# Kernel optimization log

Hardware: AMD Instinct MI355X
Metric: run time of the kernel (lower is better)

The kernel has to match this reference:

```python
import jax, jax.numpy as jnp
import numpy as np

D_MODEL = 2048
N_HEADS = 8
N_KV = 4
HEAD_DIM = 256
WINDOW = 1024
EPS = 1e-6
ROPE_BASE = 10000.0


def _rms_norm(x, w):
    # x: [..., D]; matches torch: x * rsqrt(mean(x^2) + eps) * w
    return x * jax.lax.rsqrt(jnp.mean(x * x, axis=-1, keepdims=True) + EPS) * w


def _rope_cos_sin(pos):
    # pos: [T] ints -> cos/sin: [T, HEAD_DIM] (cat(freqs, freqs) as in source)
    inv_freq = 1.0 / (ROPE_BASE ** (jnp.arange(0, HEAD_DIM, 2, dtype=jnp.float32) / HEAD_DIM))
    freqs = pos.astype(jnp.float32)[:, None] * inv_freq[None, :]  # [T, D/2]
    emb = jnp.concatenate([freqs, freqs], axis=-1)                # [T, D]
    return jnp.cos(emb), jnp.sin(emb)


def _apply_rotary(x, cos, sin):
    # x: [B, H, T, D]; interleaved rotate-half exactly as the torch code
    x1 = x[..., 0::2]
    x2 = x[..., 1::2]
    x_rot = jnp.stack([-x2, x1], axis=-1).reshape(x.shape)
    return x * cos[None, None, :, :] + x_rot * sin[None, None, :, :]


def setup_inputs() -> dict:
    key = jax.random.key(0)
    ks = jax.random.split(key, 8)
    B, T = 1, 4096
    s = 0.02
    return {
        "x": jax.random.normal(ks[0], (B, T, D_MODEL), dtype=jnp.float32),
        "pos": jnp.arange(T, dtype=jnp.int32),
        "Wq": jax.random.normal(ks[1], (N_HEADS * HEAD_DIM, D_MODEL), dtype=jnp.float32) * s,
        "Wk": jax.random.normal(ks[2], (N_KV * HEAD_DIM, D_MODEL), dtype=jnp.float32) * s,
        "Wv": jax.random.normal(ks[3], (N_KV * HEAD_DIM, D_MODEL), dtype=jnp.float32) * s,
        "Wo": jax.random.normal(ks[4], (D_MODEL, N_HEADS * HEAD_DIM), dtype=jnp.float32) * s,
        "q_norm_w": jnp.ones((HEAD_DIM,), dtype=jnp.float32),
        "k_norm_w": jnp.ones((HEAD_DIM,), dtype=jnp.float32),
    }


def reference(x, pos, Wq, Wk, Wv, Wo, q_norm_w, k_norm_w):
    B, T, _ = x.shape
    # projections (torch Linear: y = x @ W.T)
    q = (x @ Wq.T).reshape(B, T, N_HEADS, HEAD_DIM).transpose(0, 2, 1, 3)  # [B,H,T,D]
    k = (x @ Wk.T).reshape(B, T, N_KV, HEAD_DIM).transpose(0, 2, 1, 3)    # [B,Hkv,T,D]
    v = (x @ Wv.T).reshape(B, T, N_KV, HEAD_DIM).transpose(0, 2, 1, 3)
    # per-head RMSNorm
    q = _rms_norm(q, q_norm_w)
    k = _rms_norm(k, k_norm_w)
    # RoPE
    cos, sin = _rope_cos_sin(pos)
    q = _apply_rotary(q, cos, sin)
    k = _apply_rotary(k, cos, sin)
    # GQA repeat: [B,Hkv,T,D] -> [B,H,T,D]
    rep = N_HEADS // N_KV
    k = jnp.repeat(k, rep, axis=1)
    v = jnp.repeat(v, rep, axis=1)
    # full scores + sliding-window causal mask (faithful to source)
    scores = jnp.einsum("bhqd,bhkd->bhqk", q, k) / jnp.sqrt(jnp.float32(HEAD_DIM))
    i = jnp.arange(T)[:, None]
    j = jnp.arange(T)[None, :]
    allowed = (j <= i) & (j >= i - WINDOW + 1)  # [T,T]
    scores = jnp.where(allowed[None, None, :, :], scores, -jnp.inf)
    attn = jax.nn.softmax(scores, axis=-1)
    y = jnp.einsum("bhqk,bhkd->bhqd", attn, v)
    y = y.transpose(0, 2, 1, 3).reshape(B, T, N_HEADS * HEAD_DIM)
    return y @ Wo.T
```

## Files before the change

kernel.cpp:

```cpp
#include <hip/hip_runtime.h>
#include <cstdint>
#include <cmath>

typedef __bf16 bf16x8 __attribute__((ext_vector_type(8)));
typedef float  f32x4  __attribute__((ext_vector_type(4)));

#define DEVI __device__ __forceinline__

#define SEQ 4096
#define NH 8
#define NKV 4
#define HD 256
#define WIN 1024

DEVI void gload16(const void* g, void* l) {
  __builtin_amdgcn_global_load_lds((const __attribute__((address_space(1))) void*)g,
                                   (__attribute__((address_space(3))) void*)l,
                                   16, 0, 0);
}

DEVI bf16x8 ld8f(const float* p) {
  const f32x4 a = *(const f32x4*)p;
  const f32x4 b = *(const f32x4*)(p + 4);
  bf16x8 r;
#pragma unroll
  for (int j = 0; j < 4; ++j) { r[j] = (__bf16)a[j]; r[4 + j] = (__bf16)b[j]; }
  return r;
}

DEVI void st1(float* p, float v)  { *p = v; }
DEVI void st1(__bf16* p, float v) { *p = (__bf16)v; }

DEVI void barx() {
  asm volatile("" ::: "memory");
  __builtin_amdgcn_s_barrier();
  asm volatile("" ::: "memory");
}

__global__ __launch_bounds__(256)
void cvt_all(const float* __restrict__ x,  const float* __restrict__ wq,
             const float* __restrict__ wk, const float* __restrict__ wv,
             const float* __restrict__ wo,
             __bf16* __restrict__ xb, __bf16* __restrict__ wqkvb,
             __bf16* __restrict__ wob) {
  const size_t g = (size_t)blockIdx.x * 256 + threadIdx.x;
  const float* src; __bf16* dst; size_t off;
  if      (g < 1048576) { src = x;  dst = xb;               off = g; }
  else if (g < 1572864) { src = wq; dst = wqkvb;            off = g - 1048576; }
  else if (g < 1835008) { src = wk; dst = wqkvb + 4194304;  off = g - 1572864; }
  else if (g < 2097152) { src = wv; dst = wqkvb + 6291456;  off = g - 1835008; }
  else                  { src = wo; dst = wob;              off = g - 2097152; }
  *(bf16x8*)(dst + off * 8) = ld8f(src + off * 8);
}

template <int BM, typename TC>
__global__ __launch_bounds__(512, 2)
void gemm256(const __bf16* __restrict__ A, const __bf16* __restrict__ B,
             TC* __restrict__ C, int N, int K) {
  constexpr int AI    = BM / 128;
  constexpr int MF    = BM / 32;
  constexpr int MH    = MF / 2;
  constexpr int AUNIT = BM * 64;
  constexpr int ASZ   = 4 * AUNIT;
  constexpr int VMC   = 2 * AI + 4;
  __shared__ char lds[ASZ + 65536];

  const int tid  = threadIdx.x;
  const int lane = tid & 63;
  const int wave = tid >> 6;
  const int l15  = lane & 15;
  const int l4   = lane >> 4;
  const int wm   = wave >> 2;
  const int wn   = wave & 3;

  constexpr int nTm = 4096 / BM;
  const int lin  = blockIdx.x;
  const int xcd  = lin & 7;
  const int kk   = lin >> 3;
  const int nTn  = N >> 8;
  const int rowT = kk % nTm;
  const int colT = xcd * (nTn >> 3) + kk / nTm;
  const int row0 = rowT * BM;
  const int col0 = colT << 8;

  const int srow = tid >> 2;
  const int scol = ((tid & 3) ^ ((tid >> 3) & 3)) << 3;
  const __bf16* Asrc = A + (size_t)(row0 + srow) * K + scol;
  const __bf16* Bsrc = B + (size_t)(col0 + srow) * K + scol;

  const int swz  = (l4 ^ ((l15 >> 1) & 3)) << 4;
  const int aoff = (wm * (BM / 2) + l15) * 64 + swz;
  const int boff = ((wn << 6) + l15) * 64 + swz;

  auto stA = [&](int kx, int h) {
    int k0 = kx << 6; if (k0 >= K) k0 = 0;
    const __bf16* s = Asrc + k0 + (h << 5);
    char* d = lds + ((kx & 1) * 2 + h) * AUNIT + wave * 1024;
#pragma unroll
    for (int i = 0; i < AI; ++i)
      gload16(s + (size_t)(i << 7) * K, d + i * 8192);
  };
  auto stB = [&](int kx, int h) {
    int k0 = kx << 6; if (k0 >= K) k0 = 0;
    const __bf16* s = Bsrc + k0 + (h << 5);
    char* d = lds + ASZ + ((kx & 1) * 2 + h) * 16384 + wave * 1024;
#pragma unroll
    for (int i = 0; i < 2; ++i)
      gload16(s + (size_t)(i << 7) * K, d + i * 8192);
  };

  f32x4 acc[MF][4] = {};

  stA(0, 0); stB(0, 0); stA(0, 1); stB(0, 1); stA(1, 0); stB(1, 0);
  asm volatile("s_waitcnt vmcnt(%0)" :: "i"(VMC) : "memory");
  barx();

  const int NT = K >> 6;
  for (int kt = 0; kt < NT; ++kt) {
    const int bb = (kt & 1) * 2;
    bf16x8 bfr[4];
    bf16x8 af[MH];

    auto rd = [&](int h, int mg, bool readB) {
      const char* pa = lds + (bb + h) * AUNIT + aoff;
#pragma unroll
      for (int m = 0; m < MH; ++m)
        af[m] = *(const bf16x8*)(pa + ((mg * MH + m) << 10));
      if (readB) {
        const char* pb = lds + ASZ + (bb + h) * 16384 + boff;
#pragma unroll
        for (int n = 0; n < 4; ++n)
          bfr[n] = *(const bf16x8*)(pb + (n << 10));
      }
    };
    auto mm = [&](int mg) {
      barx();
      __builtin_amdgcn_s_setprio(1);
#pragma unroll
      for (int m = 0; m < MH; ++m)
#pragma unroll
        for (int n = 0; n < 4; ++n)
          acc[mg * MH + m][n] =
              __builtin_amdgcn_mfma_f32_16x16x32_bf16(af[m], bfr[n], acc[mg * MH + m][n], 0, 0, 0);
      __builtin_amdgcn_s_setprio(0);
    };

    rd(0, 0, true);
    stA(kt + 1, 1);
    mm(0);
    rd(0, 1, false);
    stB(kt + 1, 1);
    asm volatile("s_waitcnt vmcnt(%0)" :: "i"(VMC) : "memory");
    mm(1);
    rd(1, 0, true);
    stA(kt + 2, 0);
    mm(0);
    rd(1, 1, false);
    stB(kt + 2, 0);
    asm volatile("s_waitcnt vmcnt(%0)" :: "i"(VMC) : "memory");
    mm(1);
  }
  asm volatile("s_waitcnt vmcnt(0)" ::: "memory");

#pragma unroll
  for (int mf = 0; mf < MF; ++mf) {
    const int rb = row0 + wm * (BM / 2) + (mf >> 2) * 64 + (mf & 3) * 16 + (l4 << 2);
#pragma unroll
    for (int reg = 0; reg < 4; ++reg) {
      TC* crow = C + (size_t)(rb + reg) * N + col0 + (wn << 6) + l15;
#pragma unroll
      for (int n = 0; n < 4; ++n) st1(crow + (n << 4), acc[mf][n][reg]);
    }
  }
}

__global__ __launch_bounds__(256)
void norm_rope_tv(__bf16* __restrict__ qkv, __bf16* __restrict__ Vt,
                  const float* __restrict__ qw, const float* __restrict__ kw,
                  const int* __restrict__ pos) {
  if (blockIdx.x < 12288) {
    const int gw   = blockIdx.x * 4 + (threadIdx.x >> 6);
    const int lane = threadIdx.x & 63;
    __bf16* base; const float* w; int t;
    if (gw < SEQ * NH) {
      t = gw >> 3;
      base = qkv + (size_t)t * 4096 + (gw & 7) * HD;
      w = qw;
    } else {
      const int g = gw - SEQ * NH;
      t = g >> 2;
      base = qkv + (size_t)t * 4096 + 2048 + (g & 3) * HD;
      w = kw;
    }

    const int d0 = lane * 4;
    float v[4]; float ss = 0.f;
#pragma unroll
    for (int j = 0; j < 4; ++j) { v[j] = (float)base[d0 + j]; ss += v[j] * v[j]; }
#pragma unroll
    for (int off = 1; off < 64; off <<= 1) ss += __shfl_xor(ss, off);
    const float rms = rsqrtf(ss * (1.0f / 256.0f) + 1e-6f);
    const float p = (float)pos[t];

    float n[4];
#pragma unroll
    for (int j = 0; j < 4; ++j) n[j] = v[j] * rms * w[d0 + j];

    float outv[4];
#pragma unroll
    for (int e = 0; e < 4; e += 2) {
      const int i0 = d0 + e, i1 = i0 + 1;
      const float f0 = exp2f(-(float)(i0 & 127) * 0.103810253f);
      const float f1 = exp2f(-(float)(i1 & 127) * 0.103810253f);
      float s0, cc0, s1, cc1;
      sincosf(p * f0, &s0, &cc0);
      sincosf(p * f1, &s1, &cc1);
      outv[e]     = n[e] * cc0 - n[e + 1] * s0;
      outv[e + 1] = n[e + 1] * cc1 + n[e] * s1;
    }
#pragma unroll
    for (int j = 0; j < 4; ++j) base[d0 + j] = (__bf16)outv[j];
  } else {
    __shared__ __bf16 tile[64][72];
    const int b   = blockIdx.x - 12288;
    const int tid = threadIdx.x;
    const int tb  = (b & 63) * 64;
    const int yy  = b >> 6;
    const int kvh = yy >> 2;
    const int db  = (yy & 3) * 64;
#pragma unroll
    for (int i = 0; i < 2; ++i) {
      const int s = i * 256 + tid;
      const int r = s >> 3, c = (s & 7) * 8;
      bf16x8 val = *(const bf16x8*)(qkv + (size_t)(tb + r) * 4096 + 3072 + kvh * HD + db + c);
#pragma unroll
      for (int j = 0; j < 8; ++j) tile[r][c + j] = val[j];
    }
    __syncthreads();
#pragma unroll
    for (int i = 0; i < 2; ++i) {
      const int s = i * 256 + tid;
      const int r = s >> 3, c = (s & 7) * 8;
      bf16x8 outv;
#pragma unroll
      for (int j = 0; j < 8; ++j) outv[j] = tile[c + j][r];
      *(bf16x8*)(Vt + (size_t)(kvh * HD + db + r) * SEQ + tb + c) = outv;
    }
  }
}

__global__ __launch_bounds__(256, 2)
void attn_fwd(const __bf16* __restrict__ qkv, const __bf16* __restrict__ Vt,
              __bf16* __restrict__ Y) {
  __shared__ char klds[2][16384];
  __shared__ char vlds[2][16384];
  __shared__ __bf16 Ps[4][16][40];
  const int tid  = threadIdx.x;
  const int lane = tid & 63;
  const int wave = tid >> 6;
  const int l15  = lane & 15;
  const int l4   = lane >> 4;
  const int lin  = blockIdx.x;
  const int head = lin & 7;
  const int q0   = (lin >> 3) * 64;
  const int kvh  = head >> 1;
  const int qw   = q0 + wave * 16;

  bf16x8 qf[8];
  const __bf16* qrow = qkv + (size_t)(qw + l15) * 4096 + head * HD;
#pragma unroll
  for (int ks = 0; ks < 8; ++ks) {
    bf16x8 t = *(const bf16x8*)(qrow + ks * 32 + l4 * 8);
#pragma unroll
    for (int j = 0; j < 8; ++j) t[j] = (__bf16)((float)t[j] * 0.0625f);
    qf[ks] = t;
  }

  f32x4 o[16] = {};
  float l_run[4] = {0.f, 0.f, 0.f, 0.f};

  int lo = q0 - (WIN - 1); if (lo < 0) lo = 0;
  const int kt0 = lo >> 5;
  const int kt1 = (q0 + 63) >> 5;
  const int kbmax = kt1 << 5;

  const int skey = (tid >> 2) & 31;
  const int sdim = tid >> 2;
  const int sg   = (tid & 3) ^ ((tid >> 3) & 3);
  const int sth  = tid >> 7;

  auto stK = [&](int kt, int b) {
    int kb = kt << 5; if (kb > kbmax) kb = kbmax;
    const __bf16* s = qkv + (size_t)(kb + skey) * 4096 + 2048 + kvh * HD
                          + sth * 32 + sg * 8;
    char* d = klds[b] + wave * 1024;
#pragma unroll
    for (int i = 0; i < 4; ++i)
      gload16(s + i * 64, d + i * 4096);
  };
  auto stV = [&](int kt, int b) {
    int kb = kt << 5; if (kb > kbmax) kb = kbmax;
    const __bf16* s = Vt + ((size_t)kvh * HD + sdim) * SEQ + kb + sg * 8;
    char* d = vlds[b] + wave * 1024;
#pragma unroll
    for (int i = 0; i < 4; ++i)
      gload16(s + (size_t)i * 64 * SEQ, d + i * 4096);
  };

  stK(kt0, 0);     stV(kt0, 0);
  stK(kt0 + 1, 1); stV(kt0 + 1, 1);

  const int rswz = (l4 ^ ((l15 >> 1) & 3)) << 4;

  for (int kt = kt0; kt <= kt1; ++kt) {
    const int p  = (kt - kt0) & 1;
    const int kb = kt << 5;
    asm volatile("s_waitcnt vmcnt(8)" ::: "memory");
    barx();

    const char* kbase = klds[p];
    f32x4 s_acc[2] = {};
    __builtin_amdgcn_s_setprio(1);
#pragma unroll
    for (int kn = 0; kn < 2; ++kn) {
#pragma unroll
      for (int ks = 0; ks < 8; ++ks) {
        bf16x8 kf = *(const bf16x8*)(kbase + (ks * 32 + kn * 16 + l15) * 64 + rswz);
        s_acc[kn] = __builtin_amdgcn_mfma_f32_16x16x32_bf16(qf[ks], kf, s_acc[kn], 0, 0, 0);
      }
    }
    __builtin_amdgcn_s_setprio(0);

#pragma unroll
    for (int reg = 0; reg < 4; ++reg) {
      const int r  = l4 * 4 + reg;
      const int qg = qw + r;
      float ps = 0.f;
#pragma unroll
      for (int kn = 0; kn < 2; ++kn) {
        const int kg = kb + kn * 16 + l15;
        const bool ok = (kg <= qg) && (kg > qg - WIN);
        const float pv = ok ? __expf(fminf(s_acc[kn][reg], 34.f) - 34.f) : 0.f;
        ps += pv;
        Ps[wave][r][kn * 16 + l15] = (__bf16)pv;
      }
      l_run[reg] += ps;
    }

    const char* vbase = vlds[p];
    bf16x8 pf = *(const bf16x8*)&Ps[wave][l15][l4 * 8];
    __builtin_amdgcn_s_setprio(1);
#pragma unroll
    for (int dn = 0; dn < 16; ++dn) {
      bf16x8 vf = *(const bf16x8*)(vbase + (dn * 16 + l15) * 64 + rswz);
      o[dn] = __builtin_amdgcn_mfma_f32_16x16x32_bf16(pf, vf, o[dn], 0, 0, 0);
    }
    __builtin_amdgcn_s_setprio(0);

    barx();
    stK(kt + 2, p);
    stV(kt + 2, p);
  }
  asm volatile("s_waitcnt vmcnt(0)" ::: "memory");

#pragma unroll
  for (int reg = 0; reg < 4; ++reg) {
#pragma unroll
    for (int off = 1; off < 16; off <<= 1)
      l_run[reg] += __shfl_xor(l_run[reg], off);
    const float inv = 1.0f / l_run[reg];
    const int q = qw + l4 * 4 + reg;
    __bf16* yrow = Y + ((size_t)q * NH + head) * HD + l15;
#pragma unroll
    for (int dn = 0; dn < 16; ++dn)
      yrow[dn * 16] = (__bf16)(o[dn][reg] * inv);
  }
}

extern "C" void kernel_launch(void* const* d_in, const int* in_sizes, int n_in,
                              void* d_out, int out_size, void* d_ws, size_t ws_size,
                              hipStream_t stream) {
  (void)in_sizes; (void)n_in; (void)out_size; (void)ws_size;
  const float* x   = (const float*)d_in[0];
  const int*   pos = (const int*)d_in[1];
  const float* Wq  = (const float*)d_in[2];
  const float* Wk  = (const float*)d_in[3];
  const float* Wv  = (const float*)d_in[4];
  const float* Wo  = (const float*)d_in[5];
  const float* qw  = (const float*)d_in[6];
  const float* kw  = (const float*)d_in[7];
  float* out = (float*)d_out;

  char* ws = (char*)d_ws;
  const size_t MB = 1024 * 1024;
  __bf16* qkv_ws = (__bf16*)(ws);
  __bf16* vt_ws  = (__bf16*)(ws + 32 * MB);
  __bf16* y_ws   = (__bf16*)(ws + 40 * MB);
  __bf16* xb     = (__bf16*)(ws + 56 * MB);
  __bf16* wqkvb  = (__bf16*)(ws + 72 * MB);
  __bf16* wob    = (__bf16*)(ws + 88 * MB);

  cvt_all<<<dim3(10240), dim3(256), 0, stream>>>(x, Wq, Wk, Wv, Wo, xb, wqkvb, wob);
  gemm256<256, __bf16><<<dim3(256), dim3(512), 0, stream>>>(xb, wqkvb, qkv_ws, 4096, 2048);
  norm_rope_tv<<<dim3(13312), dim3(256), 0, stream>>>(qkv_ws, vt_ws, qw, kw, pos);
  attn_fwd<<<dim3(512), dim3(256), 0, stream>>>(qkv_ws, vt_ws, y_ws);
  gemm256<128, float><<<dim3(256), dim3(512), 0, stream>>>(y_ws, wob, out, 2048, 2048);
}
```

Measured before the change: 324.9 us.

## Software-pipeline QK scores in attention and add two-phase pipelined output GEMM

The attention loop now computes the next tile's QK^T scores before processing the current tile's softmax and PV, with K prefetch issued earlier. The score MFMA chains are split into independent accumulators to shorten dependency latency. A new GEMM kernel with half-K-tile double buffering and launch bounds allowing two blocks per CU replaces the output projection GEMM. This trades extra registers and LDS staging for more overlap of memory loads with MFMA work.

Result: faster. 312.5 us (-3.8%).

```diff
diff --git a/kernel.cpp b/kernel.cpp
--- a/kernel.cpp
+++ b/kernel.cpp
@@ -161,6 +161,116 @@
     mm(1);
   }
   asm volatile("s_waitcnt vmcnt(0)" ::: "memory");
+
+#pragma unroll
+  for (int mf = 0; mf < MF; ++mf) {
+    const int rb = row0 + wm * (BM / 2) + (mf >> 2) * 64 + (mf & 3) * 16 + (l4 << 2);
+#pragma unroll
+    for (int reg = 0; reg < 4; ++reg) {
+      TC* crow = C + (size_t)(rb + reg) * N + col0 + (wn << 6) + l15;
+#pragma unroll
+      for (int n = 0; n < 4; ++n) st1(crow + (n << 4), acc[mf][n][reg]);
+    }
+  }
+}
+
+template <int BM, typename TC>
+__global__ __launch_bounds__(512, 2)
+void gemm2ph(const __bf16* __restrict__ A, const __bf16* __restrict__ B,
+             TC* __restrict__ C, int N, int K) {
+  constexpr int AI    = BM / 128;
+  constexpr int MF    = BM / 32;
+  constexpr int AUNIT = BM * 64;
+  constexpr int ASZ   = 4 * AUNIT;
+  constexpr int VMC   = 2 * (AI + 2);
+  __shared__ char lds[ASZ + 65536];
+
+  const int tid  = threadIdx.x;
+  const int lane = tid & 63;
+  const int wave = tid >> 6;
+  const int l15  = lane & 15;
+  const int l4   = lane >> 4;
+  const int wm   = wave >> 2;
+  const int wn   = wave & 3;
+
+  constexpr int nTm = 4096 / BM;
+  const int lin  = blockIdx.x;
+  const int xcd  = lin & 7;
+  const int kk   = lin >> 3;
+  const int nTn  = N >> 8;
+  const int rowT = kk % nTm;
+  const int colT = xcd * (nTn >> 3) + kk / nTm;
+  const int row0 = rowT * BM;
+  const int col0 = colT << 8;
+
+  const int srow = tid >> 2;
+  const int scol = ((tid & 3) ^ ((tid >> 3) & 3)) << 3;
+  const __bf16* Asrc = A + (size_t)(row0 + srow) * K + scol;
+  const __bf16* Bsrc = B + (size_t)(col0 + srow) * K + scol;
+
+  const int swz  = (l4 ^ ((l15 >> 1) & 3)) << 4;
+  const int aoff = (wm * (BM / 2) + l15) * 64 + swz;
+  const int boff = ((wn << 6) + l15) * 64 + swz;
+
+  auto stA = [&](int kx, int h, int b) {
+    int k0 = kx << 6; if (k0 >= K) k0 = 0;
+    const __bf16* s = Asrc + k0 + (h << 5);
+    char* d = lds + (b * 2 + h) * AUNIT + wave * 1024;
+#pragma unroll
+    for (int i = 0; i < AI; ++i)
+      gload16(s + (size_t)(i << 7) * K, d + i * 8192);
+  };
+  auto stB = [&](int kx, int h, int b) {
+    int k0 = kx << 6; if (k0 >= K) k0 = 0;
+    const __bf16* s = Bsrc + k0 + (h << 5);
+    char* d = lds + ASZ + (b * 2 + h) * 16384 + wave * 1024;
+#pragma unroll
+    for (int i = 0; i < 2; ++i)
+      gload16(s + (size_t)(i << 7) * K, d + i * 8192);
+  };
+
+  f32x4 acc[MF][4] = {};
+
+  stA(0, 0, 0); stB(0, 0, 0);
+  stA(0, 1, 0); stB(0, 1, 0);
+  stA(1, 0, 1); stB(1, 0, 1);
+
+  const int NT = K >> 6;
+  for (int kt = 0; kt < NT; ++kt) {
+    const int b = kt & 1, nb = b ^ 1;
+#pragma unroll
+    for (int half = 0; half < 2; ++half) {
+      asm volatile("s_waitcnt vmcnt(%0)" :: "i"(VMC) : "memory");
+      barx();
+      bf16x8 af[4], ag[4], bfr[4];
+      const char* pa = lds + (b * 2 + half) * AUNIT + aoff;
+      const char* pb = lds + ASZ + (b * 2 + half) * 16384 + boff;
+#pragma unroll
+      for (int m = 0; m < 4; ++m) af[m] = *(const bf16x8*)(pa + (m << 10));
+#pragma unroll
+      for (int n = 0; n < 4; ++n) bfr[n] = *(const bf16x8*)(pb + (n << 10));
+      if constexpr (BM == 256) {
+#pragma unroll
+        for (int m = 0; m < 4; ++m) ag[m] = *(const bf16x8*)(pa + 4096 + (m << 10));
+      }
+      if (half == 0) { stA(kt + 1, 1, nb); stB(kt + 1, 1, nb); }
+      else           { stA(kt + 2, 0, b);  stB(kt + 2, 0, b);  }
+      __builtin_amdgcn_s_setprio(1);
+#pragma unroll
+      for (int m = 0; m < 4; ++m)
+#pragma unroll
+        for (int n = 0; n < 4; ++n)
+          acc[m][n] = __builtin_amdgcn_mfma_f32_16x16x32_bf16(af[m], bfr[n], acc[m][n], 0, 0, 0);
+      if constexpr (BM == 256) {
+#pragma unroll
+        for (int m = 0; m < 4; ++m)
+#pragma unroll
+          for (int n = 0; n < 4; ++n)
+            acc[4 + m][n] = __builtin_amdgcn_mfma_f32_16x16x32_bf16(ag[m], bfr[n], acc[4 + m][n], 0, 0, 0);
+      }
+      __builtin_amdgcn_s_setprio(0);
+    }
+  }
 
 #pragma unroll
   for (int mf = 0; mf < MF; ++mf) {
@@ -307,29 +417,48 @@
       gload16(s + (size_t)i * 64 * SEQ, d + i * 4096);
   };
 
+  const int rswz = (l4 ^ ((l15 >> 1) & 3)) << 4;
+
+  auto computeS = [&](const char* kbase, f32x4* s) {
+    f32x4 a0 = {}, a1 = {}, b0 = {}, b1 = {};
+    __builtin_amdgcn_s_setprio(1);
+#pragma unroll
+    for (int ks = 0; ks < 4; ++ks) {
+      bf16x8 k0 = *(const bf16x8*)(kbase + (ks * 32 + l15) * 64 + rswz);
+      bf16x8 k1 = *(const bf16x8*)(kbase + (ks * 32 + 16 + l15) * 64 + rswz);
+      a0 = __builtin_amdgcn_mfma_f32_16x16x32_bf16(qf[ks], k0, a0, 0, 0, 0);
+      b0 = __builtin_amdgcn_mfma_f32_16x16x32_bf16(qf[ks], k1, b0, 0, 0, 0);
+    }
+#pragma unroll
+    for (int ks = 4; ks < 8; ++ks) {
+      bf16x8 k0 = *(const bf16x8*)(kbase + (ks * 32 + l15) * 64 + rswz);
+      bf16x8 k1 = *(const bf16x8*)(kbase + (ks * 32 + 16 + l15) * 64 + rswz);
+      a1 = __builtin_amdgcn_mfma_f32_16x16x32_bf16(qf[ks], k0, a1, 0, 0, 0);
+      b1 = __builtin_amdgcn_mfma_f32_16x16x32_bf16(qf[ks], k1, b1, 0, 0, 0);
+    }
+    __builtin_amdgcn_s_setprio(0);
+    s[0] = a0 + a1;
+    s[1] = b0 + b1;
+  };
+
   stK(kt0, 0);     stV(kt0, 0);
   stK(kt0 + 1, 1); stV(kt0 + 1, 1);
-
-  const int rswz = (l4 ^ ((l15 >> 1) & 3)) << 4;
+  asm volatile("s_waitcnt vmcnt(12)" ::: "memory");
+  barx();
+  f32x4 sc[2];
+  computeS(klds[0], sc);
 
   for (int kt = kt0; kt <= kt1; ++kt) {
-    const int p  = (kt - kt0) & 1;
+    const int p  = (kt - kt0) & 1, np = p ^ 1;
     const int kb = kt << 5;
-    asm volatile("s_waitcnt vmcnt(8)" ::: "memory");
+
+    asm volatile("s_waitcnt vmcnt(4)" ::: "memory");
     barx();
 
-    const char* kbase = klds[p];
-    f32x4 s_acc[2] = {};
-    __builtin_amdgcn_s_setprio(1);
-#pragma unroll
-    for (int kn = 0; kn < 2; ++kn) {
-#pragma unroll
-      for (int ks = 0; ks < 8; ++ks) {
-        bf16x8 kf = *(const bf16x8*)(kbase + (ks * 32 + kn * 16 + l15) * 64 + rswz);
-        s_acc[kn] = __builtin_amdgcn_mfma_f32_16x16x32_bf16(qf[ks], kf, s_acc[kn], 0, 0, 0);
-      }
-    }
-    __builtin_amdgcn_s_setprio(0);
+    stK(kt + 2, p);
+
+    f32x4 sn[2];
+    computeS(klds[np], sn);
 
 #pragma unroll
     for (int reg = 0; reg < 4; ++reg) {
@@ -340,7 +469,7 @@
       for (int kn = 0; kn < 2; ++kn) {
         const int kg = kb + kn * 16 + l15;
         const bool ok = (kg <= qg) && (kg > qg - WIN);
-        const float pv = ok ? __expf(fminf(s_acc[kn][reg], 34.f) - 34.f) : 0.f;
+        const float pv = ok ? __expf(fminf(sc[kn][reg], 34.f) - 34.f) : 0.f;
         ps += pv;
         Ps[wave][r][kn * 16 + l15] = (__bf16)pv;
       }
@@ -358,8 +487,8 @@
     __builtin_amdgcn_s_setprio(0);
 
     barx();
-    stK(kt + 2, p);
     stV(kt + 2, p);
+    sc[0] = sn[0]; sc[1] = sn[1];
   }
   asm volatile("s_waitcnt vmcnt(0)" ::: "memory");
 
@@ -404,5 +533,5 @@
   gemm256<256, __bf16><<<dim3(256), dim3(512), 0, stream>>>(xb, wqkvb, qkv_ws, 4096, 2048);
   norm_rope_tv<<<dim3(13312), dim3(256), 0, stream>>>(qkv_ws, vt_ws, qw, kw, pos);
   attn_fwd<<<dim3(512), dim3(256), 0, stream>>>(qkv_ws, vt_ws, y_ws);
-  gemm256<128, float><<<dim3(256), dim3(512), 0, stream>>>(y_ws, wob, out, 2048, 2048);
-}
+  gemm2ph<128, float><<<dim3(256), dim3(512), 0, stream>>>(y_ws, wob, out, 2048, 2048);
+}
```
